# Performance work log

Hardware: AMD Instinct MI355X
Metric: run time of the kernel (lower is better)

Reference implementation:

```python
import jax, jax.numpy as jnp
import numpy as np

N = 32768          # B*T flattened tokens
E = 1024           # embed_dim
H = 16             # num_heads
D = E // H         # head_dim = 64


def setup_inputs() -> dict:
    key = jax.random.key(0)
    ks = jax.random.split(key, 9)
    w = lambda k: jax.random.normal(k, (E, E), jnp.float32) * (E ** -0.5)
    b = lambda k: jax.random.normal(k, (E,), jnp.float32) * 0.01
    return {
        "x": jax.random.normal(ks[0], (N, E), jnp.float32),
        "Wq": w(ks[1]), "bq": b(ks[2]),
        "Wk": w(ks[3]), "bk": b(ks[4]),
        "Wv": w(ks[5]), "bv": b(ks[6]),
        "Wo": w(ks[7]), "bo": b(ks[8]),
    }


def reference(x, Wq, bq, Wk, bk, Wv, bv, Wo, bo):
    # nn.Linear: y = x @ W^T + b
    q = (x @ Wq.T + bq).reshape(-1, H, D)   # [N, H, D]
    k = (x @ Wk.T + bk).reshape(-1, H, D)
    v = (x @ Wv.T + bv).reshape(-1, H, D)
    scale = D ** -0.5
    # per-token attention ACROSS HEADS: scores [N, H, H]
    qk = jnp.einsum('nhd,nHd->nhH', q, k) * scale
    attn = jax.nn.softmax(qk, axis=-1)      # softmax over key-heads
    out = jnp.einsum('nhH,nHd->nhd', attn, v).reshape(-1, E)
    return out @ Wo.T + bo                  # [N, E]
```

## Files before the change

### kernel.cpp

```cpp
#include <hip/hip_runtime.h>

typedef __attribute__((ext_vector_type(8))) short short8;
typedef __attribute__((ext_vector_type(8))) unsigned short ushort8;
typedef __attribute__((ext_vector_type(4))) float f32x4;

__device__ __forceinline__ float b2f(short s) {
    unsigned u = ((unsigned)(unsigned short)s) << 16;
    return __builtin_bit_cast(float, u);
}
__device__ __forceinline__ unsigned short f2b(float f) {
    unsigned u = __builtin_bit_cast(unsigned, f);
    u += 0x7fffu + ((u >> 16) & 1u);
    return (unsigned short)(u >> 16);
}

__device__ __forceinline__ void gload_lds16(const void* gptr, void* ldsptr) {
    typedef __attribute__((address_space(1))) const void gv_t;
    typedef __attribute__((address_space(3))) void lv_t;
    gv_t* g = reinterpret_cast<gv_t*>(reinterpret_cast<unsigned long long>(gptr));
    lv_t* l = reinterpret_cast<lv_t*>((unsigned int)reinterpret_cast<unsigned long long>(ldsptr));
    __builtin_amdgcn_global_load_lds(g, l, 16, 0, 0);
}

#define MEMFENCE() asm volatile("" ::: "memory")
#define BARRIER() do { MEMFENCE(); __builtin_amdgcn_s_barrier(); MEMFENCE(); } while (0)
#define LGKM0() do { asm volatile("s_waitcnt lgkmcnt(0)" ::: "memory"); __builtin_amdgcn_sched_barrier(0); } while (0)
#define LGKM8() do { asm volatile("s_waitcnt lgkmcnt(8)" ::: "memory"); __builtin_amdgcn_sched_barrier(0); } while (0)

__global__ __launch_bounds__(256) void cvt_bf16(const float* __restrict__ in,
                                                unsigned short* __restrict__ out,
                                                int n8) {
    int i = blockIdx.x * 256 + threadIdx.x;
    if (i >= n8) return;
    const float4* p = (const float4*)in + (size_t)i * 2;
    float4 a = p[0], b = p[1];
    ushort8 o;
    o[0] = f2b(a.x); o[1] = f2b(a.y); o[2] = f2b(a.z); o[3] = f2b(a.w);
    o[4] = f2b(b.x); o[5] = f2b(b.y); o[6] = f2b(b.z); o[7] = f2b(b.w);
    *(ushort8*)(out + (size_t)i * 8) = o;
}

__global__ __launch_bounds__(256) void concat3(const float* __restrict__ a,
                                               const float* __restrict__ b,
                                               const float* __restrict__ c,
                                               float* __restrict__ o) {
    int i = blockIdx.x * 256 + threadIdx.x;
    float v = (i < 1024) ? a[i] : (i < 2048 ? b[i - 1024] : c[i - 2048]);
    o[i] = v;
}

template <bool OUT_BF16>
__global__ __launch_bounds__(512, 2) void gemm_bt(const short* __restrict__ A,
                                                  const short* __restrict__ B,
                                                  const float* __restrict__ bias,
                                                  unsigned short* __restrict__ Cb,
                                                  float* __restrict__ Cf,
                                                  int M, int N, int K) {
    extern __shared__ short lds[];
    short* Ab = lds;
    short* Bb = lds + 2 * 2 * 128 * 64;

    const int lane = threadIdx.x & 63;
    const int wave = threadIdx.x >> 6;
    const int wr = wave >> 2;
    const int wc = wave & 3;

    const int nwg = gridDim.x;
    const int bid = blockIdx.x;
    const int swz = (bid & 7) * (nwg >> 3) + (bid >> 3);
    const int ncol = N >> 8;
    const int trow = swz / ncol, tcol = swz % ncol;

    const short* Ablk = A + (size_t)trow * 256 * K;
    const short* Bblk = B + (size_t)tcol * 256 * K;

    const int scol_sw = ((lane & 7) ^ (lane >> 3)) * 8;
    const int rl = lane & 15;
    const int g0 = (((lane >> 4)) ^ (lane & 7)) * 8;
    const int g1 = ((4 + (lane >> 4)) ^ (lane & 7)) * 8;

    short8 af[8][2];
    short8 bf[4];
    f32x4 acc[8][4] = {};

    const int NT = K >> 6;
    const int smax = 4 * (NT - 2);

    auto stage_half = [&](int ts, int h) {
        const int dd = ts & 1;
        const int hh = h & 1;
        const short* gb = ((h < 2) ? Ablk : Bblk) + (size_t)(hh * 128) * K + (ts << 6) + scol_sw;
        short* lb = ((h < 2) ? Ab : Bb) + (((dd << 1) | hh) << 13);
#pragma unroll
        for (int c = 0; c < 2; ++c) {
            const int row = c * 64 + wave * 8 + (lane >> 3);
            gload_lds16(gb + (size_t)row * K, lb + ((c * 64 + wave * 8) << 6));
        }
    };
    auto stage_if = [&](int s) { if (s >= 0 && s < smax) stage_half((s >> 2) + 2, s & 3); };

    auto readA = [&](int d, int ks) {
        const short* base = Ab + ((((d << 1) | wr) << 13)) + (ks ? g1 : g0);
#pragma unroll
        for (int m = 0; m < 8; ++m)
            af[m][ks] = *(const short8*)(base + ((m * 16 + rl) << 6));
    };
    auto readB = [&](int d, int ks, int np) {
        const short* base = Bb + ((((d << 1) | (wc >> 1)) << 13)) + (((wc & 1) * 64) << 6) + (ks ? g1 : g0);
#pragma unroll
        for (int j = 0; j < 2; ++j)
            bf[np * 2 + j] = *(const short8*)(base + (((np * 2 + j) * 16 + rl) << 6));
    };
    auto mmq = [&](int ks, int np) {
        __builtin_amdgcn_s_setprio(1);
#pragma unroll
        for (int m = 0; m < 8; ++m) {
            acc[m][np * 2]     = __builtin_amdgcn_mfma_f32_16x16x32_bf16(af[m][ks], bf[np * 2],     acc[m][np * 2], 0, 0, 0);
            acc[m][np * 2 + 1] = __builtin_amdgcn_mfma_f32_16x16x32_bf16(af[m][ks], bf[np * 2 + 1], acc[m][np * 2 + 1], 0, 0, 0);
        }
        __builtin_amdgcn_s_setprio(0);
    };

#pragma unroll
    for (int t = 0; t < 2; ++t)
#pragma unroll
        for (int h = 0; h < 4; ++h) stage_half(t, h);
    asm volatile("s_waitcnt vmcnt(8)" ::: "memory");
    BARRIER();

#pragma unroll 2
    for (int T = 0; T < NT; ++T) {
        const int d = T & 1;
        const int s0 = 4 * T;
        stage_if(s0 - 3);
        readA(d, 0); readB(d, 0, 0);
        LGKM0();
        mmq(0, 0);
        BARRIER();
        stage_if(s0 - 2);
        readB(d, 0, 1); readA(d, 1);
        LGKM8();
        mmq(0, 1);
        BARRIER();
        stage_if(s0 - 1);
        readB(d, 1, 0);
        LGKM0();
        mmq(1, 0);
        BARRIER();
        stage_if(s0);
        readB(d, 1, 1);
        LGKM0();
        mmq(1, 1);
        if (T < NT - 2)       asm volatile("s_waitcnt vmcnt(2)" ::: "memory");
        else if (T == NT - 2) asm volatile("s_waitcnt vmcnt(0)" ::: "memory");
        BARRIER();
    }

    const int crow0 = trow * 256 + wr * 128 + (lane >> 4) * 4;
    const int ccol0 = tcol * 256 + wc * 64 + rl;
#pragma unroll
    for (int n = 0; n < 4; ++n) {
        const int col = ccol0 + n * 16;
        const float bv = bias[col];
#pragma unroll
        for (int m = 0; m < 8; ++m) {
            const int row0 = crow0 + m * 16;
#pragma unroll
            for (int r = 0; r < 4; ++r) {
                float val = acc[m][n][r] + bv;
                if (OUT_BF16) Cb[(size_t)(row0 + r) * N + col] = f2b(val);
                else          Cf[(size_t)(row0 + r) * N + col] = val;
            }
        }
    }
}

__global__ __launch_bounds__(256) void attn_k(const short* __restrict__ qkv,
                                              short* __restrict__ out) {
    int gid = blockIdx.x * 256 + threadIdx.x;
    int t = gid >> 4, h = gid & 15;
    const short* q  = qkv + (size_t)t * 3072 + h * 64;
    const short* kb = qkv + (size_t)t * 3072 + 1024;
    const short* vb = qkv + (size_t)t * 3072 + 2048;

    float qf[64];
#pragma unroll
    for (int j = 0; j < 8; ++j) {
        short8 qv = *(const short8*)(q + j * 8);
#pragma unroll
        for (int i = 0; i < 8; ++i) qf[j * 8 + i] = b2f(qv[i]);
    }

    float s[16];
    float mx = -1e30f;
#pragma unroll
    for (int g = 0; g < 16; ++g) {
        float a = 0.f;
#pragma unroll
        for (int j = 0; j < 8; ++j) {
            short8 kv = *(const short8*)(kb + g * 64 + j * 8);
#pragma unroll
            for (int i = 0; i < 8; ++i) a += qf[j * 8 + i] * b2f(kv[i]);
        }
        s[g] = a * 0.125f;
        mx = fmaxf(mx, s[g]);
    }
    float den = 0.f;
#pragma unroll
    for (int g = 0; g < 16; ++g) { s[g] = __expf(s[g] - mx); den += s[g]; }
    float inv = 1.f / den;

#pragma unroll
    for (int j = 0; j < 8; ++j) {
        float o[8] = {0.f, 0.f, 0.f, 0.f, 0.f, 0.f, 0.f, 0.f};
#pragma unroll
        for (int g = 0; g < 16; ++g) {
            short8 vv = *(const short8*)(vb + g * 64 + j * 8);
            float w = s[g];
#pragma unroll
            for (int i = 0; i < 8; ++i) o[i] += w * b2f(vv[i]);
        }
        short8 ov;
#pragma unroll
        for (int i = 0; i < 8; ++i) ov[i] = (short)f2b(o[i] * inv);
        *(short8*)(out + (size_t)t * 1024 + h * 64 + j * 8) = ov;
    }
}

extern "C" void kernel_launch(void* const* d_in, const int* in_sizes, int n_in,
                              void* d_out, int out_size, void* d_ws, size_t ws_size,
                              hipStream_t stream) {
    const float* x  = (const float*)d_in[0];
    const float* Wq = (const float*)d_in[1];
    const float* bq = (const float*)d_in[2];
    const float* Wk = (const float*)d_in[3];
    const float* bk = (const float*)d_in[4];
    const float* Wv = (const float*)d_in[5];
    const float* bv = (const float*)d_in[6];
    const float* Wo = (const float*)d_in[7];
    const float* bo = (const float*)d_in[8];
    float* out = (float*)d_out;

    const int N = 32768, E = 1024;
    const int LDS_BYTES = 131072;

    (void)hipFuncSetAttribute((const void*)gemm_bt<true>,  hipFuncAttributeMaxDynamicSharedMemorySize, LDS_BYTES);
    (void)hipFuncSetAttribute((const void*)gemm_bt<false>, hipFuncAttributeMaxDynamicSharedMemorySize, LDS_BYTES);

    char* ws = (char*)d_ws;
    size_t off = 0;
    short* xb = (short*)(ws + off);         off += (size_t)N * E * 2;
    short* wqkv = (short*)(ws + off);       off += (size_t)3 * E * E * 2;
    short* wo = (short*)(ws + off);         off += (size_t)E * E * 2;
    float* bqkv = (float*)(ws + off);       off += (size_t)3 * E * 4;
    off = (off + 255) & ~(size_t)255;
    short* y1 = (short*)(ws + off);         off += (size_t)N * 3 * E * 2;
    short* ao = xb;

    cvt_bf16<<<dim3((N * E / 8 + 255) / 256), dim3(256), 0, stream>>>(x, (unsigned short*)xb, N * E / 8);
    cvt_bf16<<<dim3((E * E / 8 + 255) / 256), dim3(256), 0, stream>>>(Wq, (unsigned short*)wqkv, E * E / 8);
    cvt_bf16<<<dim3((E * E / 8 + 255) / 256), dim3(256), 0, stream>>>(Wk, (unsigned short*)(wqkv + (size_t)E * E), E * E / 8);
    cvt_bf16<<<dim3((E * E / 8 + 255) / 256), dim3(256), 0, stream>>>(Wv, (unsigned short*)(wqkv + (size_t)2 * E * E), E * E / 8);
    cvt_bf16<<<dim3((E * E / 8 + 255) / 256), dim3(256), 0, stream>>>(Wo, (unsigned short*)wo, E * E / 8);
    concat3<<<dim3(12), dim3(256), 0, stream>>>(bq, bk, bv, bqkv);

    gemm_bt<true><<<dim3((N / 256) * (3 * E / 256)), dim3(512), LDS_BYTES, stream>>>(
        xb, wqkv, bqkv, (unsigned short*)y1, nullptr, N, 3 * E, E);

    attn_k<<<dim3(N * 16 / 256), dim3(256), 0, stream>>>(y1, ao);

    gemm_bt<false><<<dim3((N / 256) * (E / 256)), dim3(512), LDS_BYTES, stream>>>(
        ao, wo, bo, nullptr, out, N, E, E);
}
```

Baseline: 484.0 us.

## Restructure GEMM K-loop into M/N quadrant phases with split LDS reads

Reorganizes the per-tile MFMA schedule from k-slice-major quarters to M-half/N-half quadrants, each consuming both k-sub-slices. A and B fragments are read in halves (af[4][2], bf[4][2]), which cuts fragment register use, and the LDS reads are issued before the global-to-LDS stage with extra barriers and waitcnt placement. The loop is manually unrolled by two so the double-buffer index is a constant. This is meant to reduce register pressure and improve overlap of LDS reads with MFMA, but the extra barriers add synchronization cost.

```diff
diff --git a/kernel.cpp b/kernel.cpp
--- a/kernel.cpp
+++ b/kernel.cpp
@@ -24,8 +24,6 @@
 
 #define MEMFENCE() asm volatile("" ::: "memory")
 #define BARRIER() do { MEMFENCE(); __builtin_amdgcn_s_barrier(); MEMFENCE(); } while (0)
-#define LGKM0() do { asm volatile("s_waitcnt lgkmcnt(0)" ::: "memory"); __builtin_amdgcn_sched_barrier(0); } while (0)
-#define LGKM8() do { asm volatile("s_waitcnt lgkmcnt(8)" ::: "memory"); __builtin_amdgcn_sched_barrier(0); } while (0)
 
 __global__ __launch_bounds__(256) void cvt_bf16(const float* __restrict__ in,
                                                 unsigned short* __restrict__ out,
@@ -79,8 +77,8 @@
     const int g0 = (((lane >> 4)) ^ (lane & 7)) * 8;
     const int g1 = ((4 + (lane >> 4)) ^ (lane & 7)) * 8;
 
-    short8 af[8][2];
-    short8 bf[4];
+    short8 af[4][2];
+    short8 bf[4][2];
     f32x4 acc[8][4] = {};
 
     const int NT = K >> 6;
@@ -99,26 +97,62 @@
     };
     auto stage_if = [&](int s) { if (s >= 0 && s < smax) stage_half((s >> 2) + 2, s & 3); };
 
-    auto readA = [&](int d, int ks) {
-        const short* base = Ab + ((((d << 1) | wr) << 13)) + (ks ? g1 : g0);
-#pragma unroll
-        for (int m = 0; m < 8; ++m)
-            af[m][ks] = *(const short8*)(base + ((m * 16 + rl) << 6));
-    };
-    auto readB = [&](int d, int ks, int np) {
-        const short* base = Bb + ((((d << 1) | (wc >> 1)) << 13)) + (((wc & 1) * 64) << 6) + (ks ? g1 : g0);
-#pragma unroll
-        for (int j = 0; j < 2; ++j)
-            bf[np * 2 + j] = *(const short8*)(base + (((np * 2 + j) * 16 + rl) << 6));
-    };
-    auto mmq = [&](int ks, int np) {
+    auto readA = [&](int d, int mh) {
+        const short* base = Ab + (((d << 1) | wr) << 13) + ((mh * 64 + rl) << 6);
+#pragma unroll
+        for (int m = 0; m < 4; ++m) {
+            af[m][0] = *(const short8*)(base + ((m * 16) << 6) + g0);
+            af[m][1] = *(const short8*)(base + ((m * 16) << 6) + g1);
+        }
+    };
+    auto readB = [&](int d, int nh) {
+        const short* base = Bb + (((d << 1) | (wc >> 1)) << 13) + (((wc & 1) * 64 + rl) << 6);
+#pragma unroll
+        for (int j = 0; j < 2; ++j) {
+            bf[nh * 2 + j][0] = *(const short8*)(base + (((nh * 2 + j) * 16) << 6) + g0);
+            bf[nh * 2 + j][1] = *(const short8*)(base + (((nh * 2 + j) * 16) << 6) + g1);
+        }
+    };
+    auto mm = [&](int mh, int nh) {
         __builtin_amdgcn_s_setprio(1);
 #pragma unroll
-        for (int m = 0; m < 8; ++m) {
-            acc[m][np * 2]     = __builtin_amdgcn_mfma_f32_16x16x32_bf16(af[m][ks], bf[np * 2],     acc[m][np * 2], 0, 0, 0);
-            acc[m][np * 2 + 1] = __builtin_amdgcn_mfma_f32_16x16x32_bf16(af[m][ks], bf[np * 2 + 1], acc[m][np * 2 + 1], 0, 0, 0);
-        }
+        for (int ks = 0; ks < 2; ++ks)
+#pragma unroll
+            for (int m = 0; m < 4; ++m)
+#pragma unroll
+                for (int j = 0; j < 2; ++j)
+                    acc[mh * 4 + m][nh * 2 + j] = __builtin_amdgcn_mfma_f32_16x16x32_bf16(
+                        af[m][ks], bf[nh * 2 + j][ks], acc[mh * 4 + m][nh * 2 + j], 0, 0, 0);
         __builtin_amdgcn_s_setprio(0);
+    };
+
+    auto tile_body = [&](int T, int d) {
+        const int s0 = 4 * T;
+        readA(d, 0); readB(d, 0);
+        stage_if(s0 - 3);
+        asm volatile("s_waitcnt lgkmcnt(8)" ::: "memory");
+        BARRIER();
+        asm volatile("s_waitcnt lgkmcnt(0)" ::: "memory");
+        mm(0, 0);
+        BARRIER();
+        readB(d, 1);
+        stage_if(s0 - 2);
+        BARRIER();
+        asm volatile("s_waitcnt lgkmcnt(0)" ::: "memory");
+        mm(0, 1);
+        BARRIER();
+        readA(d, 1);
+        stage_if(s0 - 1);
+        BARRIER();
+        asm volatile("s_waitcnt lgkmcnt(0)" ::: "memory");
+        mm(1, 0);
+        BARRIER();
+        stage_if(s0);
+        BARRIER();
+        mm(1, 1);
+        if (T < NT - 2)       asm volatile("s_waitcnt vmcnt(2)" ::: "memory");
+        else if (T == NT - 2) asm volatile("s_waitcnt vmcnt(0)" ::: "memory");
+        BARRIER();
     };
 
 #pragma unroll
@@ -128,32 +162,9 @@
     asm volatile("s_waitcnt vmcnt(8)" ::: "memory");
     BARRIER();
 
-#pragma unroll 2
-    for (int T = 0; T < NT; ++T) {
-        const int d = T & 1;
-        const int s0 = 4 * T;
-        stage_if(s0 - 3);
-        readA(d, 0); readB(d, 0, 0);
-        LGKM0();
-        mmq(0, 0);
-        BARRIER();
-        stage_if(s0 - 2);
-        readB(d, 0, 1); readA(d, 1);
-        LGKM8();
-        mmq(0, 1);
-        BARRIER();
-        stage_if(s0 - 1);
-        readB(d, 1, 0);
-        LGKM0();
-        mmq(1, 0);
-        BARRIER();
-        stage_if(s0);
-        readB(d, 1, 1);
-        LGKM0();
-        mmq(1, 1);
-        if (T < NT - 2)       asm volatile("s_waitcnt vmcnt(2)" ::: "memory");
-        else if (T == NT - 2) asm volatile("s_waitcnt vmcnt(0)" ::: "memory");
-        BARRIER();
+    for (int T2 = 0; T2 < NT; T2 += 2) {
+        tile_body(T2, 0);
+        tile_body(T2 + 1, 1);
     }
 
     const int crow0 = trow * 256 + wr * 128 + (lane >> 4) * 4;
```

Result: no change. 478.0 us (-1.2%).
